# Kernel tuning notes

Measured on AMD Instinct MI355X. Metric: run time of the kernel, lower is better.

## Reference

```python
import jax, jax.numpy as jnp
import numpy as np

K = 65536          # memory bank size
P = 4096           # partition_size
D = 256            # out_dim
E = 2              # num_experts_per_concept
SMOOTH = 0.1
NUM_TASKS = 1
B = 4096


def setup_inputs() -> dict:
    key = jax.random.key(0)
    k1, k2, k3 = jax.random.split(key, 3)
    queue = jax.random.normal(k1, (D, K), dtype=jnp.float32)
    queue = queue / jnp.linalg.norm(queue, axis=0, keepdims=True)  # normalize(dim=0)
    return {
        "student_embeds": jax.random.normal(k2, (B, D), dtype=jnp.float32),
        "teacher_embeds": jax.random.normal(k3, (B, D), dtype=jnp.float32),
        "queue": queue,
        "student_temp": 0.1,
        "teacher_temp": 0.04,
    }


def _one_task(queue, student_embeds, teacher_embeds, student_temp, teacher_temp, key):
    kperm, ksel = jax.random.split(key)
    # random partition of the bank (torch.randperm + split)
    perm = jax.random.permutation(kperm, K)
    part_idx, mem_idx = perm[:P], perm[P:]
    part = queue[:, part_idx]                      # [D, P]
    mem = queue[:, mem_idx]                        # [D, K-P]
    Kmp = K - P

    sims = part.T @ mem                            # [P, K-P]
    neigh_scores, neigh_idx = jax.lax.top_k(sims, E - 1)  # [P, E-1]

    # append self index (offset into concatenated [mem | part]) and 1-smoothing score
    idx_ = jnp.concatenate([neigh_idx, (Kmp + jnp.arange(P))[:, None]], axis=1)          # [P, E]
    scores_ = jnp.concatenate(
        [neigh_scores, jnp.full((P, 1), 1.0 - SMOOTH, dtype=sims.dtype)], axis=1)        # [P, E]

    # low_energy selection: multinomial(weights, P//2, replacement=False)
    P2 = P // 2
    m = jnp.mean(neigh_scores, axis=-1)            # [P]
    sample_means = jnp.abs(m)
    sample_stds = m                                 # (faithful to source: same quantity)
    coef = (sample_stds / (sample_means + 1e-8)) * (1.0 + 1.0 / (4.0 * Kmp))
    weights = 1.0 / coef                            # [P]
    # Gumbel top-k == multinomial without replacement proportional to weights
    gumbel = jax.random.gumbel(ksel, (P,))
    sel = jax.lax.top_k(jnp.log(weights) + gumbel, P2)[1]   # [P2]
    idx_ = idx_[sel]                                # [P2, E]
    scores_ = scores_[sel]                          # [P2, E]

    embeds_ = jnp.concatenate([mem, part], axis=1)  # [D, K]
    pne = embeds_[:, idx_.reshape(-1)]              # [D, P2*E] partition_neigh_embeddings

    sf = scores_.reshape(-1)                        # [P2*E]
    smooth_val = (1.0 - sf) / (P2 - 1)              # [P2*E]
    # partition_labels = arange(P).repeat_interleave(E)[:P2*E] == repeat(arange(P2), E)
    labels = jnp.repeat(jnp.arange(P2), E)          # [P2*E]
    M = jnp.broadcast_to(smooth_val[:, None], (P2 * E, P2))
    M = M.at[jnp.arange(P2 * E), labels].set(sf)    # scatter_ on dim 1
    M = M / M.sum(-1, keepdims=True)                # row-normalize

    s_probs = jax.nn.softmax(student_embeds @ pne / student_temp, axis=-1) @ M  # [B, P2]
    t_probs = jax.nn.softmax(teacher_embeds @ pne / teacher_temp, axis=-1) @ M  # [B, P2]
    return s_probs, t_probs


def reference(student_embeds, teacher_embeds, queue, student_temp, teacher_temp):
    base = jax.random.key(42)  # internal RNG (torch.randperm / multinomial equivalents)
    s_list, t_list = [], []
    for i in range(NUM_TASKS):
        s, t = _one_task(queue, student_embeds, teacher_embeds,
                         student_temp, teacher_temp, jax.random.fold_in(base, i))
        s_list.append(s)
        t_list.append(t)
    return jnp.stack(s_list), jnp.stack(t_list)  # each [NUM_TASKS, B, P//2]
```

## Files before the change

kernel.cpp:

```cpp
#include <hip/hip_runtime.h>
#include <cstdint>
#include <cmath>
#include <cstring>
#include <vector>
#include <algorithm>
#include <utility>

#define KTOT 65536
#define PP   4096
#define DD   256
#define KMP  61440
#define P2   2048
#define BB   4096
#define NPB  512
#define INVALID_C 0xFFFFFFFFu

static inline void tf2x32(uint32_t k0, uint32_t k1, uint32_t x0, uint32_t x1,
                          uint32_t* o0, uint32_t* o1) {
  static const uint32_t rot[2][4] = {{13u,15u,26u,6u},{17u,29u,16u,24u}};
  uint32_t ks[3] = {k0, k1, 0x1BD11BDAu ^ k0 ^ k1};
  uint32_t v0 = x0 + ks[0], v1 = x1 + ks[1];
  for (int i = 0; i < 5; ++i) {
    const uint32_t* r = rot[i & 1];
    for (int j = 0; j < 4; ++j) {
      v0 += v1;
      v1 = (v1 << r[j]) | (v1 >> (32u - r[j]));
      v1 ^= v0;
    }
    v0 += ks[(i + 1) % 3];
    v1 += ks[(i + 2) % 3] + (uint32_t)(i + 1);
  }
  *o0 = v0; *o1 = v1;
}

static inline uint32_t tf_bits32(uint32_t k0, uint32_t k1, uint32_t i) {
  uint32_t a, b;
  tf2x32(k0, k1, 0u, i, &a, &b);
  return a ^ b;
}

static uint32_t h_upload[KMP + KTOT + P2];
static uint32_t* const h_mem_idx    = h_upload;
static uint32_t* const h_pos_in_mem = h_upload + KMP;
static uint32_t* const h_partsel    = h_upload + KMP + KTOT;

static void host_prepare() {
  uint32_t f0, f1; tf2x32(0u, 42u, 0u, 0u, &f0, &f1);
  uint32_t kperm0, kperm1, ksel0, ksel1;
  tf2x32(f0, f1, 0u, 0u, &kperm0, &kperm1);
  tf2x32(f0, f1, 0u, 1u, &ksel0, &ksel1);

  std::vector<uint32_t> perm(KTOT);
  for (uint32_t i = 0; i < KTOT; ++i) perm[i] = i;
  std::vector<std::pair<uint32_t,uint32_t>> kv(KTOT);
  uint32_t key0 = kperm0, key1 = kperm1;
  for (int round = 0; round < 2; ++round) {
    uint32_t nk0, nk1, sk0, sk1;
    tf2x32(key0, key1, 0u, 0u, &nk0, &nk1);
    tf2x32(key0, key1, 0u, 1u, &sk0, &sk1);
    key0 = nk0; key1 = nk1;
    for (uint32_t i = 0; i < KTOT; ++i) {
      kv[i].first  = tf_bits32(sk0, sk1, i);
      kv[i].second = perm[i];
    }
    std::stable_sort(kv.begin(), kv.end(),
        [](const std::pair<uint32_t,uint32_t>& a,
           const std::pair<uint32_t,uint32_t>& b){ return a.first < b.first; });
    for (uint32_t i = 0; i < KTOT; ++i) perm[i] = kv[i].second;
  }
  static uint32_t part_idx[PP];
  for (int i = 0; i < PP;  ++i) part_idx[i] = perm[i];
  for (int i = 0; i < KMP; ++i) h_mem_idx[i] = perm[PP + i];
  for (int i = 0; i < KTOT; ++i) h_pos_in_mem[i] = INVALID_C;
  for (uint32_t c = 0; c < KMP; ++c) h_pos_in_mem[h_mem_idx[c]] = c;

  static float sval[PP];
  float c1f = (float)(1.0 + 1.0/(4.0*(double)KMP));
  float L0  = logf(1.0f / c1f);
  for (uint32_t i = 0; i < PP; ++i) {
    uint32_t bits = tf_bits32(ksel0, ksel1, i);
    uint32_t fb = (bits >> 9) | 0x3F800000u;
    float f; memcpy(&f, &fb, 4);
    f -= 1.0f;
    float u = (f == 0.0f) ? 1.17549435e-38f : f;
    float g = -logf(-logf(u));
    sval[i] = L0 + g;
  }
  static uint32_t order[PP];
  for (uint32_t i = 0; i < PP; ++i) order[i] = i;
  std::sort(order, order + PP, [](uint32_t a, uint32_t b){
    if (sval[a] != sval[b]) return sval[a] > sval[b];
    return a < b;
  });
  for (int k = 0; k < P2; ++k) h_partsel[k] = part_idx[order[k]];

  (void)hipHostRegister((void*)h_upload, sizeof(h_upload), hipHostRegisterDefault);
}

static const bool _host_tables_ready = (host_prepare(), true);

typedef __attribute__((ext_vector_type(8))) short bf16x8;
typedef __attribute__((ext_vector_type(4))) float f32x4;

__device__ inline unsigned short f2bf(float x) {
  union { float f; uint32_t u; } v; v.f = x;
  return (unsigned short)((v.u + 0x7FFFu + ((v.u >> 16) & 1u)) >> 16);
}

__device__ inline void gload16(const unsigned short* g, unsigned short* l) {
  __builtin_amdgcn_global_load_lds(
      (const __attribute__((address_space(1))) unsigned int*)g,
      (__attribute__((address_space(3))) unsigned int*)l, 16, 0, 0);
}

__device__ inline float wave_max(float v) {
#pragma unroll
  for (int off = 32; off > 0; off >>= 1) v = fmaxf(v, __shfl_xor(v, off, 64));
  return v;
}
__device__ inline float wave_sum(float v) {
#pragma unroll
  for (int off = 32; off > 0; off >>= 1) v += __shfl_xor(v, off, 64);
  return v;
}

__device__ __host__ inline int swz_g(int row) {
  return ((row >> 1) & 3) | (((row >> 3) & 1) << 3);
}
__device__ __host__ inline int swz(int row, int d) {
  return d ^ (swz_g(row) << 1);
}

__global__ __launch_bounds__(256)
void transpose_bf16(const float* __restrict__ queue, unsigned short* __restrict__ BhT) {
  __shared__ float t[64][65];
  const int tid = threadIdx.x;
  const int c4 = (tid & 15) * 4, r = tid >> 4;
  const int n0 = blockIdx.x * 64, d0 = blockIdx.y * 64;
#pragma unroll
  for (int i = 0; i < 4; ++i) {
    int d = r + i * 16;
    float4 v = *(const float4*)&queue[(d0 + d) * KTOT + n0 + c4];
    t[d][c4 + 0] = v.x; t[d][c4 + 1] = v.y; t[d][c4 + 2] = v.z; t[d][c4 + 3] = v.w;
  }
  __syncthreads();
#pragma unroll
  for (int i = 0; i < 4; ++i) {
    int n = r + i * 16;
    uint32_t lo = (uint32_t)f2bf(t[c4 + 0][n]) | ((uint32_t)f2bf(t[c4 + 1][n]) << 16);
    uint32_t hi = (uint32_t)f2bf(t[c4 + 2][n]) | ((uint32_t)f2bf(t[c4 + 3][n]) << 16);
    const int row = n0 + n;
    const int g = swz_g(row);
    const int pos = ((d0 + c4) ^ (g << 1)) & ~3;
    uint2 w;
    w.x = (g & 1) ? hi : lo;
    w.y = (g & 1) ? lo : hi;
    *(uint2*)&BhT[row * DD + pos] = w;
  }
}

__global__ __launch_bounds__(256)
void gather_A(const float* __restrict__ queue, const uint32_t* __restrict__ psel,
              float* __restrict__ Apart, unsigned short* __restrict__ AhT) {
  int p = blockIdx.x, d = threadIdx.x;
  float q = queue[d * KTOT + (int)psel[p]];
  Apart[p * DD + d] = q;
  AhT[p * DD + swz(p, d)] = f2bf(q);
}

__global__ __launch_bounds__(256)
void mfma_argmax(const unsigned short* __restrict__ AhT,
                 const unsigned short* __restrict__ BhT,
                 const uint32_t* __restrict__ pos_in_mem,
                 float* __restrict__ pv2, uint32_t* __restrict__ pc2) {
  __shared__ union SM {
    struct { unsigned short As[2][128][32]; unsigned short Bs[2][128][32]; } s;
    struct { float rv[128][33]; uint32_t ri[128][33]; } r;
  } sm;
  const int tid = threadIdx.x;

  const int flat = blockIdx.y * NPB + blockIdx.x;
  const int xcd = flat & 7, job = flat >> 3;
  const int nt = (xcd << 6) + (job >> 4);
  const int mt = job & 15;
  const int m0 = mt * 128, n0 = nt * 128;

  const int wave = tid >> 6, lane = tid & 63;
  const int wm = (wave >> 1) * 64, wn = (wave & 1) * 64;
  const int l15 = lane & 15, quad = lane >> 4;

  uint32_t carr[4];
#pragma unroll
  for (int j = 0; j < 4; ++j) carr[j] = pos_in_mem[n0 + wn + j * 16 + l15];

  const int gsw = swz_g(l15);
  const int o0 = (((quad << 2) | 0) ^ gsw) << 2;
  const int o1 = (((quad << 2) | 1) ^ gsw) << 2;
  const int o2 = (((quad << 2) | 2) ^ gsw) << 2;
  const int o3 = (((quad << 2) | 3) ^ gsw) << 2;

  f32x4 acc[4][4];
#pragma unroll
  for (int i = 0; i < 4; ++i)
#pragma unroll
    for (int j = 0; j < 4; ++j) acc[i][j] = (f32x4){0.f, 0.f, 0.f, 0.f};

  const int r4 = lane >> 2;
  const int c8 = (lane & 3) * 8;
  const unsigned short* gA0 = &AhT[(m0 + wave * 16 + r4) * DD + c8];
  const unsigned short* gA1 = gA0 + 64 * DD;
  const unsigned short* gB0 = &BhT[(n0 + wave * 16 + r4) * DD + c8];
  const unsigned short* gB1 = gB0 + 64 * DD;

  {
    unsigned short* lA = &sm.s.As[0][wave * 16][0];
    unsigned short* lB = &sm.s.Bs[0][wave * 16][0];
    gload16(gA0, lA); gload16(gA1, lA + 64 * 32);
    gload16(gB0, lB); gload16(gB1, lB + 64 * 32);
  }
  __syncthreads();

#pragma unroll
  for (int t = 0; t < 8; ++t) {
    const int cur = t & 1;
    if (t < 7) {
      const int k0 = (t + 1) * 32;
      unsigned short* lA = &sm.s.As[cur ^ 1][wave * 16][0];
      unsigned short* lB = &sm.s.Bs[cur ^ 1][wave * 16][0];
      gload16(gA0 + k0, lA); gload16(gA1 + k0, lA + 64 * 32);
      gload16(gB0 + k0, lB); gload16(gB1 + k0, lB + 64 * 32);
    }
    bf16x8 a[4], b[4];
#pragma unroll
    for (int i = 0; i < 4; ++i) {
      const char* rb = (const char*)&sm.s.As[cur][wm + i * 16 + l15][0];
      union { uint32_t u[4]; bf16x8 v; } f;
      f.u[0] = *(const uint32_t*)(rb + o0);
      f.u[1] = *(const uint32_t*)(rb + o1);
      f.u[2] = *(const uint32_t*)(rb + o2);
      f.u[3] = *(const uint32_t*)(rb + o3);
      a[i] = f.v;
    }
#pragma unroll
    for (int j = 0; j < 4; ++j) {
      const char* rb = (const char*)&sm.s.Bs[cur][wn + j * 16 + l15][0];
      union { uint32_t u[4]; bf16x8 v; } f;
      f.u[0] = *(const uint32_t*)(rb + o0);
      f.u[1] = *(const uint32_t*)(rb + o1);
      f.u[2] = *(const uint32_t*)(rb + o2);
      f.u[3] = *(const uint32_t*)(rb + o3);
      b[j] = f.v;
    }
#pragma unroll
    for (int i = 0; i < 4; ++i)
#pragma unroll
      for (int j = 0; j < 4; ++j)
        acc[i][j] = __builtin_amdgcn_mfma_f32_16x16x32_bf16(a[i], b[j], acc[i][j], 0, 0, 0);
    __syncthreads();
  }

#pragma unroll
  for (int i = 0; i < 4; ++i)
#pragma unroll
    for (int r = 0; r < 4; ++r) {
      float bv = -INFINITY; uint32_t bc = INVALID_C;
#pragma unroll
      for (int j = 0; j < 4; ++j) {
        float v = acc[i][j][r]; uint32_t c = carr[j];
        if (c != INVALID_C && (v > bv || (v == bv && c < bc))) { bv = v; bc = c; }
      }
      int row = wm + i * 16 + quad * 4 + r;
      sm.r.rv[row][(wave & 1) * 16 + l15] = bv;
      sm.r.ri[row][(wave & 1) * 16 + l15] = bc;
    }
  __syncthreads();
  if (tid < 128) {
    float v1 = -INFINITY, v2 = -INFINITY; uint32_t c1 = INVALID_C, c2 = INVALID_C;
#pragma unroll 4
    for (int s = 0; s < 32; ++s) {
      float v = sm.r.rv[tid][s]; uint32_t c = sm.r.ri[tid][s];
      if (c == INVALID_C) continue;
      if (v > v1 || (v == v1 && c < c1)) { v2 = v1; c2 = c1; v1 = v; c1 = c; }
      else if (v > v2 || (v == v2 && c < c2)) { v2 = v; c2 = c; }
    }
    int base = (m0 + tid) * (NPB * 2) + nt * 2;
    pv2[base] = v1;     pc2[base] = c1;
    pv2[base + 1] = v2; pc2[base + 1] = c2;
  }
}

#define EPS_W 0.01f
__global__ __launch_bounds__(256)
void argmax_rescore(const float* __restrict__ pv2, const uint32_t* __restrict__ pc2,
                    const float* __restrict__ Apart, const float* __restrict__ queue,
                    const uint32_t* __restrict__ mem_idx,
                    float* __restrict__ nval, uint32_t* __restrict__ nc) {
  __shared__ float wr[4];
  __shared__ uint32_t cand[32];
  __shared__ int cnt;
  __shared__ float bestv_s; __shared__ uint32_t bestc_s;
  const int row = blockIdx.x, tid = threadIdx.x;
  const int wave = tid >> 6;

  if (tid == 0) { cnt = 0; bestv_s = -INFINITY; bestc_s = INVALID_C; }
  float m = -INFINITY;
  for (int e = tid; e < NPB * 2; e += 256) m = fmaxf(m, pv2[row * (NPB * 2) + e]);
  m = wave_max(m);
  if ((tid & 63) == 0) wr[wave] = m;
  __syncthreads();
  const float M = fmaxf(fmaxf(wr[0], wr[1]), fmaxf(wr[2], wr[3]));
  for (int e = tid; e < NPB * 2; e += 256) {
    float v = pv2[row * (NPB * 2) + e]; uint32_t c = pc2[row * (NPB * 2) + e];
    if (c != INVALID_C && v >= M - EPS_W) {
      int k = atomicAdd(&cnt, 1);
      if (k < 32) cand[k] = c;
    }
  }
  __syncthreads();
  const int ncand = min(cnt, 32);
  const float av = Apart[row * DD + tid];
  for (int k = 0; k < ncand; ++k) {
    uint32_t c = cand[k];
    int n = (int)mem_idx[c];
    float p = wave_sum(av * queue[tid * KTOT + n]);
    if ((tid & 63) == 0) wr[wave] = p;
    __syncthreads();
    if (tid == 0) {
      float sc = wr[0] + wr[1] + wr[2] + wr[3];
      if (sc > bestv_s || (sc == bestv_s && c < bestc_s)) { bestv_s = sc; bestc_s = c; }
    }
    __syncthreads();
  }
  if (tid == 0) { nval[row] = bestv_s; nc[row] = bestc_s; }
}

__global__ __launch_bounds__(256)
void prep(const uint32_t* __restrict__ nc, const float* __restrict__ nval,
          const uint32_t* __restrict__ mem_idx, const uint32_t* __restrict__ partsel,
          uint32_t* __restrict__ g_idx, float* __restrict__ svp, float* __restrict__ dp) {
  int k = blockIdx.x * 256 + threadIdx.x;
  if (k >= P2) return;
  uint32_t c = nc[k];
  float sf0 = nval[k];
  float sf1 = 0.9f;
  g_idx[2 * k]     = mem_idx[c];
  g_idx[2 * k + 1] = partsel[k];
  float sv0 = (1.0f - sf0) / 2047.0f;
  float sv1 = (1.0f - sf1) / 2047.0f;
  float rs0 = sf0 + 2047.0f * sv0;
  float rs1 = sf1 + 2047.0f * sv1;
  svp[2 * k]     = sv0 / rs0;  dp[2 * k]     = (sf0 - sv0) / rs0;
  svp[2 * k + 1] = sv1 / rs1;  dp[2 * k + 1] = (sf1 - sv1) / rs1;
}

__global__ __launch_bounds__(256)
void cvt_A(const float* __restrict__ S, const float* __restrict__ T,
           unsigned short* __restrict__ AhS, unsigned short* __restrict__ AlS,
           unsigned short* __restrict__ AhT, unsigned short* __restrict__ AlT) {
  int b = blockIdx.x, d = threadIdx.x;
  const float* src = (b < BB) ? S : T;
  unsigned short* oh = (b < BB) ? AhS : AhT;
  unsigned short* ol = (b < BB) ? AlS : AlT;
  int row = b & (BB - 1);
  float v = src[row * DD + d];
  unsigned short hb = f2bf(v);
  float hf = __uint_as_float((uint32_t)hb << 16);
  unsigned short lb = f2bf(v - hf);
  int o = row * DD + swz(row, d);
  oh[o] = hb;
  ol[o] = lb;
}

__global__ __launch_bounds__(256)
void gather_B(const float* __restrict__ queue, const uint32_t* __restrict__ g_idx,
              unsigned short* __restrict__ Bh, unsigned short* __restrict__ Bl) {
  int r = blockIdx.x, d = threadIdx.x;
  float v = queue[d * KTOT + (int)g_idx[r]];
  unsigned short hb = f2bf(v);
  float hf = __uint_as_float((uint32_t)hb << 16);
  unsigned short lb = f2bf(v - hf);
  int o = r * DD + swz(r, d);
  Bh[o] = hb;
  Bl[o] = lb;
}

__global__ __launch_bounds__(256)
void gemm_split(const unsigned short* __restrict__ Ah,
                const unsigned short* __restrict__ Al,
                const unsigned short* __restrict__ Bh,
                const unsigned short* __restrict__ Bl,
                float* __restrict__ Fo) {
  __shared__ struct { unsigned short As[2][128][32]; unsigned short Bs[2][128][32]; } sm;
  const int tid = threadIdx.x;
  const int m0 = blockIdx.y * 128, n0 = blockIdx.x * 128;
  const int wave = tid >> 6, lane = tid & 63;
  const int wm = (wave >> 1) * 64, wn = (wave & 1) * 64;
  const int l15 = lane & 15, quad = lane >> 4;

  const int gsw = swz_g(l15);
  const int o0 = (((quad << 2) | 0) ^ gsw) << 2;
  const int o1 = (((quad << 2) | 1) ^ gsw) << 2;
  const int o2 = (((quad << 2) | 2) ^ gsw) << 2;
  const int o3 = (((quad << 2) | 3) ^ gsw) << 2;

  f32x4 acc[4][4];
#pragma unroll
  for (int i = 0; i < 4; ++i)
#pragma unroll
    for (int j = 0; j < 4; ++j) acc[i][j] = (f32x4){0.f, 0.f, 0.f, 0.f};

  const int r4 = lane >> 2;
  const int c8 = (lane & 3) * 8;
  const int aoff = (m0 + wave * 16 + r4) * DD + c8;
  const int boff = (n0 + wave * 16 + r4) * DD + c8;

  {
    unsigned short* lA = &sm.As[0][wave * 16][0];
    unsigned short* lB = &sm.Bs[0][wave * 16][0];
    gload16(Ah + aoff, lA); gload16(Ah + aoff + 64 * DD, lA + 64 * 32);
    gload16(Bh + boff, lB); gload16(Bh + boff + 64 * DD, lB + 64 * 32);
  }
  __syncthreads();

#pragma unroll 2
  for (int t = 0; t < 24; ++t) {
    const int cur = t & 1;
    if (t < 23) {
      const int tn = t + 1;
      const int p = tn >> 3, k0 = (tn & 7) * 32;
      const unsigned short* ga = ((p == 2) ? Al : Ah) + aoff + k0;
      const unsigned short* gb = ((p == 1) ? Bl : Bh) + boff + k0;
      unsigned short* lA = &sm.As[cur ^ 1][wave * 16][0];
      unsigned short* lB = &sm.Bs[cur ^ 1][wave * 16][0];
      gload16(ga, lA); gload16(ga + 64 * DD, lA + 64 * 32);
      gload16(gb, lB); gload16(gb + 64 * DD, lB + 64 * 32);
    }
    bf16x8 a[4], b[4];
#pragma unroll
    for (int i = 0; i < 4; ++i) {
      const char* rb = (const char*)&sm.As[cur][wm + i * 16 + l15][0];
      union { uint32_t u[4]; bf16x8 v; } f;
      f.u[0] = *(const uint32_t*)(rb + o0);
      f.u[1] = *(const uint32_t*)(rb + o1);
      f.u[2] = *(const uint32_t*)(rb + o2);
      f.u[3] = *(const uint32_t*)(rb + o3);
      a[i] = f.v;
    }
#pragma unroll
    for (int j = 0; j < 4; ++j) {
      const char* rb = (const char*)&sm.Bs[cur][wn + j * 16 + l15][0];
      union { uint32_t u[4]; bf16x8 v; } f;
      f.u[0] = *(const uint32_t*)(rb + o0);
      f.u[1] = *(const uint32_t*)(rb + o1);
      f.u[2] = *(const uint32_t*)(rb + o2);
      f.u[3] = *(const uint32_t*)(rb + o3);
      b[j] = f.v;
    }
#pragma unroll
    for (int i = 0; i < 4; ++i)
#pragma unroll
      for (int j = 0; j < 4; ++j)
        acc[i][j] = __builtin_amdgcn_mfma_f32_16x16x32_bf16(a[i], b[j], acc[i][j], 0, 0, 0);
    __syncthreads();
  }

#pragma unroll
  for (int i = 0; i < 4; ++i)
#pragma unroll
    for (int j = 0; j < 4; ++j)
#pragma unroll
      for (int r = 0; r < 4; ++r)
        Fo[(m0 + wm + i * 16 + quad * 4 + r) * PP + n0 + wn + j * 16 + l15] = acc[i][j][r];
}

__global__ __launch_bounds__(256)
void softmax_out(const float* __restrict__ F, const float* __restrict__ temp_ptr,
                 const float* __restrict__ svp, const float* __restrict__ dp,
                 float* __restrict__ out) {
  __shared__ float e[PP];
  __shared__ float wrm[4], wrz[4], wrs[4];
  int b = blockIdx.x, tid = threadIdx.x;
  const int wave = tid >> 6;
  const float invtemp = 1.0f / temp_ptr[0];
  float lv[PP / 256];
  float lmax = -INFINITY;
#pragma unroll
  for (int k = 0; k < PP / 256; ++k) {
    float l = F[b * PP + tid + k * 256] * invtemp;
    lv[k] = l;
    lmax = fmaxf(lmax, l);
  }
  lmax = wave_max(lmax);
  if ((tid & 63) == 0) wrm[wave] = lmax;
  __syncthreads();
  lmax = fmaxf(fmaxf(wrm[0], wrm[1]), fmaxf(wrm[2], wrm[3]));

  float z = 0.0f, sacc = 0.0f;
#pragma unroll
  for (int k = 0; k < PP / 256; ++k) {
    int r = tid + k * 256;
    float ev = __expf(lv[k] - lmax);
    e[r] = ev;
    z += ev;
    sacc = fmaf(ev, svp[r], sacc);
  }
  z = wave_sum(z);
  sacc = wave_sum(sacc);
  if ((tid & 63) == 0) { wrz[wave] = z; wrs[wave] = sacc; }
  __syncthreads();
  z = wrz[0] + wrz[1] + wrz[2] + wrz[3];
  sacc = wrs[0] + wrs[1] + wrs[2] + wrs[3];

  float invz = 1.0f / z;
  for (int j = tid; j < P2; j += 256) {
    float v = sacc + e[2 * j] * dp[2 * j] + e[2 * j + 1] * dp[2 * j + 1];
    out[b * P2 + j] = v * invz;
  }
}

#define OFF_BHT      0u
#define OFF_PV2      33554432u
#define OFF_PC2      41943040u
#define OFF_AHT      50331648u
#define OFF_APART    51380224u
#define OFF_F        0u
#define OFF_BH       33554432u
#define OFF_BL       35651584u
#define OFF_AHS      37748736u
#define OFF_ALS      39845888u
#define OFF_AHT2     41943040u
#define OFF_ALT2     44040192u
#define OFF_SVP      71303168u
#define OFF_DP       71319552u
#define OFF_GIDX     71335936u
#define OFF_NVAL     71352320u
#define OFF_NC       71360512u
#define OFF_UP_MEM   71368704u
#define OFF_UP_POS   71614464u
#define OFF_UP_PSEL  71876608u

extern "C" void kernel_launch(void* const* d_in, const int* in_sizes, int n_in,
                              void* d_out, int out_size, void* d_ws, size_t ws_size,
                              hipStream_t stream) {
  (void)in_sizes; (void)n_in; (void)out_size; (void)ws_size;
  (void)_host_tables_ready;
  const float* d_student = (const float*)d_in[0];
  const float* d_teacher = (const float*)d_in[1];
  const float* d_queue   = (const float*)d_in[2];
  const float* d_stemp   = (const float*)d_in[3];
  const float* d_ttemp   = (const float*)d_in[4];
  float* out = (float*)d_out;
  char* ws = (char*)d_ws;

  unsigned short* BhT   = (unsigned short*)(ws + OFF_BHT);
  float*          pv2   = (float*)(ws + OFF_PV2);
  uint32_t*       pc2   = (uint32_t*)(ws + OFF_PC2);
  unsigned short* AhT   = (unsigned short*)(ws + OFF_AHT);
  float*          Apart = (float*)(ws + OFF_APART);
  float*          F     = (float*)(ws + OFF_F);
  unsigned short* Bh    = (unsigned short*)(ws + OFF_BH);
  unsigned short* Bl    = (unsigned short*)(ws + OFF_BL);
  unsigned short* AhS   = (unsigned short*)(ws + OFF_AHS);
  unsigned short* AlS   = (unsigned short*)(ws + OFF_ALS);
  unsigned short* AhT2  = (unsigned short*)(ws + OFF_AHT2);
  unsigned short* AlT2  = (unsigned short*)(ws + OFF_ALT2);
  float*          svp   = (float*)(ws + OFF_SVP);
  float*          dp    = (float*)(ws + OFF_DP);
  uint32_t*       g_idx = (uint32_t*)(ws + OFF_GIDX);
  float*          nval  = (float*)(ws + OFF_NVAL);
  uint32_t*       nc    = (uint32_t*)(ws + OFF_NC);
  uint32_t*       dMemIdx = (uint32_t*)(ws + OFF_UP_MEM);
  uint32_t*       dPosMem = (uint32_t*)(ws + OFF_UP_POS);
  uint32_t*       dPSel   = (uint32_t*)(ws + OFF_UP_PSEL);

  hipMemcpyAsync(dMemIdx, h_upload, sizeof(h_upload), hipMemcpyHostToDevice, stream);

  transpose_bf16<<<dim3(KTOT / 64, DD / 64), 256, 0, stream>>>(d_queue, BhT);
  gather_A<<<P2, 256, 0, stream>>>(d_queue, dPSel, Apart, AhT);
  mfma_argmax<<<dim3(NPB, P2 / 128), 256, 0, stream>>>(AhT, BhT, dPosMem, pv2, pc2);
  argmax_rescore<<<P2, 256, 0, stream>>>(pv2, pc2, Apart, d_queue, dMemIdx, nval, nc);
  prep<<<P2 / 256, 256, 0, stream>>>(nc, nval, dMemIdx, dPSel, g_idx, svp, dp);

  cvt_A<<<2 * BB, 256, 0, stream>>>(d_student, d_teacher, AhS, AlS, AhT2, AlT2);
  gather_B<<<PP, 256, 0, stream>>>(d_queue, g_idx, Bh, Bl);

  for (int half = 0; half < 2; ++half) {
    gemm_split<<<dim3(PP / 128, 2048 / 128), 256, 0, stream>>>(
        AhS + (size_t)half * 2048 * DD, AlS + (size_t)half * 2048 * DD, Bh, Bl, F);
    softmax_out<<<2048, 256, 0, stream>>>(F, d_stemp, svp, dp,
        out + (size_t)half * 2048 * P2);
  }
  for (int half = 0; half < 2; ++half) {
    gemm_split<<<dim3(PP / 128, 2048 / 128), 256, 0, stream>>>(
        AhT2 + (size_t)half * 2048 * DD, AlT2 + (size_t)half * 2048 * DD, Bh, Bl, F);
    softmax_out<<<2048, 256, 0, stream>>>(F, d_ttemp, svp, dp,
        out + (size_t)BB * P2 + (size_t)half * 2048 * P2);
  }
}
```

Before: 477.4 us.

## Fuse prep kernels and switch LDS swizzle to 64-bit fragment reads

Merges transpose_bf16 with gather_A, and prep, cvt_A and gather_B, into two combined kernels that branch on block index. This removes kernel launches and the g_idx intermediate buffer. The shared-memory swizzle is redefined so each MFMA operand fragment is read with two 64-bit LDS loads instead of four 32-bit loads, and the transpose write path drops its hi/lo swap. The new swizzle must stay consistent between the global writers and the LDS readers, and it may change the bank-conflict pattern.

```diff
diff --git a/kernel.cpp b/kernel.cpp
--- a/kernel.cpp
+++ b/kernel.cpp
@@ -124,48 +124,46 @@
   return v;
 }
 
-__device__ __host__ inline int swz_g(int row) {
-  return ((row >> 1) & 3) | (((row >> 3) & 1) << 3);
+__device__ __host__ inline int swz_g2(int row) {
+  return (((row >> 2) & 1) << 1) | (((row >> 3) & 1) << 3);
 }
 __device__ __host__ inline int swz(int row, int d) {
-  return d ^ (swz_g(row) << 1);
+  return d ^ (swz_g2(row) << 1);
 }
 
 __global__ __launch_bounds__(256)
-void transpose_bf16(const float* __restrict__ queue, unsigned short* __restrict__ BhT) {
-  __shared__ float t[64][65];
-  const int tid = threadIdx.x;
-  const int c4 = (tid & 15) * 4, r = tid >> 4;
-  const int n0 = blockIdx.x * 64, d0 = blockIdx.y * 64;
-#pragma unroll
-  for (int i = 0; i < 4; ++i) {
-    int d = r + i * 16;
-    float4 v = *(const float4*)&queue[(d0 + d) * KTOT + n0 + c4];
-    t[d][c4 + 0] = v.x; t[d][c4 + 1] = v.y; t[d][c4 + 2] = v.z; t[d][c4 + 3] = v.w;
-  }
-  __syncthreads();
-#pragma unroll
-  for (int i = 0; i < 4; ++i) {
-    int n = r + i * 16;
-    uint32_t lo = (uint32_t)f2bf(t[c4 + 0][n]) | ((uint32_t)f2bf(t[c4 + 1][n]) << 16);
-    uint32_t hi = (uint32_t)f2bf(t[c4 + 2][n]) | ((uint32_t)f2bf(t[c4 + 3][n]) << 16);
-    const int row = n0 + n;
-    const int g = swz_g(row);
-    const int pos = ((d0 + c4) ^ (g << 1)) & ~3;
-    uint2 w;
-    w.x = (g & 1) ? hi : lo;
-    w.y = (g & 1) ? lo : hi;
-    *(uint2*)&BhT[row * DD + pos] = w;
-  }
-}
-
-__global__ __launch_bounds__(256)
-void gather_A(const float* __restrict__ queue, const uint32_t* __restrict__ psel,
-              float* __restrict__ Apart, unsigned short* __restrict__ AhT) {
-  int p = blockIdx.x, d = threadIdx.x;
-  float q = queue[d * KTOT + (int)psel[p]];
-  Apart[p * DD + d] = q;
-  AhT[p * DD + swz(p, d)] = f2bf(q);
+void stageB_prep(const float* __restrict__ queue, const uint32_t* __restrict__ psel,
+                 unsigned short* __restrict__ BhT, float* __restrict__ Apart,
+                 unsigned short* __restrict__ AhT) {
+  const int b = blockIdx.x;
+  if (b < 4096) {
+    __shared__ float t[64][65];
+    const int tid = threadIdx.x;
+    const int c4 = (tid & 15) * 4, r = tid >> 4;
+    const int n0 = (b & 1023) * 64, d0 = (b >> 10) * 64;
+#pragma unroll
+    for (int i = 0; i < 4; ++i) {
+      int d = r + i * 16;
+      float4 v = *(const float4*)&queue[(d0 + d) * KTOT + n0 + c4];
+      t[d][c4 + 0] = v.x; t[d][c4 + 1] = v.y; t[d][c4 + 2] = v.z; t[d][c4 + 3] = v.w;
+    }
+    __syncthreads();
+#pragma unroll
+    for (int i = 0; i < 4; ++i) {
+      int n = r + i * 16;
+      uint32_t lo = (uint32_t)f2bf(t[c4 + 0][n]) | ((uint32_t)f2bf(t[c4 + 1][n]) << 16);
+      uint32_t hi = (uint32_t)f2bf(t[c4 + 2][n]) | ((uint32_t)f2bf(t[c4 + 3][n]) << 16);
+      const int row = n0 + n;
+      const int pos = (d0 + c4) ^ (swz_g2(row) << 1);
+      uint2 w; w.x = lo; w.y = hi;
+      *(uint2*)&BhT[row * DD + pos] = w;
+    }
+  } else {
+    int p = b - 4096, d = threadIdx.x;
+    float q = queue[d * KTOT + (int)psel[p]];
+    Apart[p * DD + d] = q;
+    AhT[p * DD + swz(p, d)] = f2bf(q);
+  }
 }
 
 __global__ __launch_bounds__(256)
@@ -193,11 +191,9 @@
 #pragma unroll
   for (int j = 0; j < 4; ++j) carr[j] = pos_in_mem[n0 + wn + j * 16 + l15];
 
-  const int gsw = swz_g(l15);
-  const int o0 = (((quad << 2) | 0) ^ gsw) << 2;
-  const int o1 = (((quad << 2) | 1) ^ gsw) << 2;
-  const int o2 = (((quad << 2) | 2) ^ gsw) << 2;
-  const int o3 = (((quad << 2) | 3) ^ gsw) << 2;
+  const int h64 = ((l15 >> 2) & 1) | (((l15 >> 3) & 1) << 2);
+  const int e0 = (((quad << 1) | 0) ^ h64) << 3;
+  const int e1 = (((quad << 1) | 1) ^ h64) << 3;
 
   f32x4 acc[4][4];
 #pragma unroll
@@ -234,21 +230,17 @@
 #pragma unroll
     for (int i = 0; i < 4; ++i) {
       const char* rb = (const char*)&sm.s.As[cur][wm + i * 16 + l15][0];
-      union { uint32_t u[4]; bf16x8 v; } f;
-      f.u[0] = *(const uint32_t*)(rb + o0);
-      f.u[1] = *(const uint32_t*)(rb + o1);
-      f.u[2] = *(const uint32_t*)(rb + o2);
-      f.u[3] = *(const uint32_t*)(rb + o3);
+      union { unsigned long long q[2]; bf16x8 v; } f;
+      f.q[0] = *(const unsigned long long*)(rb + e0);
+      f.q[1] = *(const unsigned long long*)(rb + e1);
       a[i] = f.v;
     }
 #pragma unroll
     for (int j = 0; j < 4; ++j) {
       const char* rb = (const char*)&sm.s.Bs[cur][wn + j * 16 + l15][0];
-      union { uint32_t u[4]; bf16x8 v; } f;
-      f.u[0] = *(const uint32_t*)(rb + o0);
-      f.u[1] = *(const uint32_t*)(rb + o1);
-      f.u[2] = *(const uint32_t*)(rb + o2);
-      f.u[3] = *(const uint32_t*)(rb + o3);
+      union { unsigned long long q[2]; bf16x8 v; } f;
+      f.q[0] = *(const unsigned long long*)(rb + e0);
+      f.q[1] = *(const unsigned long long*)(rb + e1);
       b[j] = f.v;
     }
 #pragma unroll
@@ -335,53 +327,46 @@
 }
 
 __global__ __launch_bounds__(256)
-void prep(const uint32_t* __restrict__ nc, const float* __restrict__ nval,
-          const uint32_t* __restrict__ mem_idx, const uint32_t* __restrict__ partsel,
-          uint32_t* __restrict__ g_idx, float* __restrict__ svp, float* __restrict__ dp) {
-  int k = blockIdx.x * 256 + threadIdx.x;
-  if (k >= P2) return;
-  uint32_t c = nc[k];
-  float sf0 = nval[k];
-  float sf1 = 0.9f;
-  g_idx[2 * k]     = mem_idx[c];
-  g_idx[2 * k + 1] = partsel[k];
-  float sv0 = (1.0f - sf0) / 2047.0f;
-  float sv1 = (1.0f - sf1) / 2047.0f;
-  float rs0 = sf0 + 2047.0f * sv0;
-  float rs1 = sf1 + 2047.0f * sv1;
-  svp[2 * k]     = sv0 / rs0;  dp[2 * k]     = (sf0 - sv0) / rs0;
-  svp[2 * k + 1] = sv1 / rs1;  dp[2 * k + 1] = (sf1 - sv1) / rs1;
-}
-
-__global__ __launch_bounds__(256)
-void cvt_A(const float* __restrict__ S, const float* __restrict__ T,
-           unsigned short* __restrict__ AhS, unsigned short* __restrict__ AlS,
-           unsigned short* __restrict__ AhT, unsigned short* __restrict__ AlT) {
-  int b = blockIdx.x, d = threadIdx.x;
-  const float* src = (b < BB) ? S : T;
-  unsigned short* oh = (b < BB) ? AhS : AhT;
-  unsigned short* ol = (b < BB) ? AlS : AlT;
-  int row = b & (BB - 1);
-  float v = src[row * DD + d];
-  unsigned short hb = f2bf(v);
-  float hf = __uint_as_float((uint32_t)hb << 16);
-  unsigned short lb = f2bf(v - hf);
-  int o = row * DD + swz(row, d);
-  oh[o] = hb;
-  ol[o] = lb;
-}
-
-__global__ __launch_bounds__(256)
-void gather_B(const float* __restrict__ queue, const uint32_t* __restrict__ g_idx,
-              unsigned short* __restrict__ Bh, unsigned short* __restrict__ Bl) {
-  int r = blockIdx.x, d = threadIdx.x;
-  float v = queue[d * KTOT + (int)g_idx[r]];
-  unsigned short hb = f2bf(v);
-  float hf = __uint_as_float((uint32_t)hb << 16);
-  unsigned short lb = f2bf(v - hf);
-  int o = r * DD + swz(r, d);
-  Bh[o] = hb;
-  Bl[o] = lb;
+void prep_ops(const float* __restrict__ S, const float* __restrict__ T,
+              const float* __restrict__ queue,
+              const uint32_t* __restrict__ nc, const float* __restrict__ nval,
+              const uint32_t* __restrict__ mem_idx, const uint32_t* __restrict__ partsel,
+              unsigned short* __restrict__ AhS, unsigned short* __restrict__ AlS,
+              unsigned short* __restrict__ AhT2, unsigned short* __restrict__ AlT2,
+              unsigned short* __restrict__ Bh, unsigned short* __restrict__ Bl,
+              float* __restrict__ svp, float* __restrict__ dp) {
+  const int b = blockIdx.x, d = threadIdx.x;
+  if (b < 2 * BB) {
+    const float* src = (b < BB) ? S : T;
+    unsigned short* oh = (b < BB) ? AhS : AhT2;
+    unsigned short* ol = (b < BB) ? AlS : AlT2;
+    int row = b & (BB - 1);
+    float v = src[row * DD + d];
+    unsigned short hb = f2bf(v);
+    float hf = __uint_as_float((uint32_t)hb << 16);
+    unsigned short lb = f2bf(v - hf);
+    int o = row * DD + swz(row, d);
+    oh[o] = hb;
+    ol[o] = lb;
+  } else {
+    int r = b - 2 * BB;
+    int k = r >> 1;
+    int idx = (r & 1) ? (int)partsel[k] : (int)mem_idx[nc[k]];
+    float v = queue[d * KTOT + idx];
+    unsigned short hb = f2bf(v);
+    float hf = __uint_as_float((uint32_t)hb << 16);
+    unsigned short lb = f2bf(v - hf);
+    int o = r * DD + swz(r, d);
+    Bh[o] = hb;
+    Bl[o] = lb;
+    if (!(r & 1) && d < 2) {
+      float sf = (d == 0) ? nval[k] : 0.9f;
+      float sv = (1.0f - sf) / 2047.0f;
+      float rs = sf + 2047.0f * sv;
+      svp[2 * k + d] = sv / rs;
+      dp[2 * k + d]  = (sf - sv) / rs;
+    }
+  }
 }
 
 __global__ __launch_bounds__(256)
@@ -397,11 +382,9 @@
   const int wm = (wave >> 1) * 64, wn = (wave & 1) * 64;
   const int l15 = lane & 15, quad = lane >> 4;
 
-  const int gsw = swz_g(l15);
-  const int o0 = (((quad << 2) | 0) ^ gsw) << 2;
-  const int o1 = (((quad << 2) | 1) ^ gsw) << 2;
-  const int o2 = (((quad << 2) | 2) ^ gsw) << 2;
-  const int o3 = (((quad << 2) | 3) ^ gsw) << 2;
+  const int h64 = ((l15 >> 2) & 1) | (((l15 >> 3) & 1) << 2);
+  const int e0 = (((quad << 1) | 0) ^ h64) << 3;
+  const int e1 = (((quad << 1) | 1) ^ h64) << 3;
 
   f32x4 acc[4][4];
 #pragma unroll
@@ -439,21 +422,17 @@
 #pragma unroll
     for (int i = 0; i < 4; ++i) {
       const char* rb = (const char*)&sm.As[cur][wm + i * 16 + l15][0];
-      union { uint32_t u[4]; bf16x8 v; } f;
-      f.u[0] = *(const uint32_t*)(rb + o0);
-      f.u[1] = *(const uint32_t*)(rb + o1);
-      f.u[2] = *(const uint32_t*)(rb + o2);
-      f.u[3] = *(const uint32_t*)(rb + o3);
+      union { unsigned long long q[2]; bf16x8 v; } f;
+      f.q[0] = *(const unsigned long long*)(rb + e0);
+      f.q[1] = *(const unsigned long long*)(rb + e1);
       a[i] = f.v;
     }
 #pragma unroll
     for (int j = 0; j < 4; ++j) {
       const char* rb = (const char*)&sm.Bs[cur][wn + j * 16 + l15][0];
-      union { uint32_t u[4]; bf16x8 v; } f;
-      f.u[0] = *(const uint32_t*)(rb + o0);
-      f.u[1] = *(const uint32_t*)(rb + o1);
-      f.u[2] = *(const uint32_t*)(rb + o2);
-      f.u[3] = *(const uint32_t*)(rb + o3);
+      union { unsigned long long q[2]; bf16x8 v; } f;
+      f.q[0] = *(const unsigned long long*)(rb + e0);
+      f.q[1] = *(const unsigned long long*)(rb + e1);
       b[j] = f.v;
     }
 #pragma unroll
@@ -532,7 +511,6 @@
 #define OFF_ALT2     44040192u
 #define OFF_SVP      71303168u
 #define OFF_DP       71319552u
-#define OFF_GIDX     71335936u
 #define OFF_NVAL     71352320u
 #define OFF_NC       71360512u
 #define OFF_UP_MEM   71368704u
@@ -566,7 +544,6 @@
   unsigned short* AlT2  = (unsigned short*)(ws + OFF_ALT2);
   float*          svp   = (float*)(ws + OFF_SVP);
   float*          dp    = (float*)(ws + OFF_DP);
-  uint32_t*       g_idx = (uint32_t*)(ws + OFF_GIDX);
   float*          nval  = (float*)(ws + OFF_NVAL);
   uint32_t*       nc    = (uint32_t*)(ws + OFF_NC);
   uint32_t*       dMemIdx = (uint32_t*)(ws + OFF_UP_MEM);
@@ -575,14 +552,12 @@
 
   hipMemcpyAsync(dMemIdx, h_upload, sizeof(h_upload), hipMemcpyHostToDevice, stream);
 
-  transpose_bf16<<<dim3(KTOT / 64, DD / 64), 256, 0, stream>>>(d_queue, BhT);
-  gather_A<<<P2, 256, 0, stream>>>(d_queue, dPSel, Apart, AhT);
+  stageB_prep<<<4096 + P2, 256, 0, stream>>>(d_queue, dPSel, BhT, Apart, AhT);
   mfma_argmax<<<dim3(NPB, P2 / 128), 256, 0, stream>>>(AhT, BhT, dPosMem, pv2, pc2);
   argmax_rescore<<<P2, 256, 0, stream>>>(pv2, pc2, Apart, d_queue, dMemIdx, nval, nc);
-  prep<<<P2 / 256, 256, 0, stream>>>(nc, nval, dMemIdx, dPSel, g_idx, svp, dp);
-
-  cvt_A<<<2 * BB, 256, 0, stream>>>(d_student, d_teacher, AhS, AlS, AhT2, AlT2);
-  gather_B<<<PP, 256, 0, stream>>>(d_queue, g_idx, Bh, Bl);
+
+  prep_ops<<<2 * BB + PP, 256, 0, stream>>>(d_student, d_teacher, d_queue,
+      nc, nval, dMemIdx, dPSel, AhS, AlS, AhT2, AlT2, Bh, Bl, svp, dp);
 
   for (int half = 0; half < 2; ++half) {
     gemm_split<<<dim3(PP / 128, 2048 / 128), 256, 0, stream>>>(
```

Measured after the change: 482.6 us. About the same (+1.1%).
